# Kernel optimization log

Hardware: AMD Instinct MI355X
Metric: run time of the kernel (lower is better)

Reference implementation:

```python
import jax, jax.numpy as jnp
import numpy as np

B, D, C, NS = 4, 64, 16, 4          # batch (clusters), spatial size, nPlanes (constant mode), num_strides
LEAK, EPS = 0.0, 1e-4               # leakiness_enc, SCN BatchNorm eps
N = 200_000                          # total points across clusters
DN = ('NCDHW', 'DHWIO', 'NCDHW')


def _conv(x, w, stride=1, pad='SAME'):
    return jax.lax.conv_general_dilated(x, w, (stride,) * 3, pad, dimension_numbers=DN)


def _bn_lrelu(x, m, gamma, beta):
    # BatchNormLeakyReLU over ACTIVE sites only (mask m is {0,1} float [B,1,d,d,d])
    n = jnp.maximum(jnp.sum(m), 1.0)
    mean = jnp.sum(x * m, axis=(0, 2, 3, 4)) / n
    xc = x - mean[None, :, None, None, None]
    var = jnp.sum((xc * xc) * m, axis=(0, 2, 3, 4)) / n
    xh = xc * jax.lax.rsqrt(var + EPS)[None, :, None, None, None]
    xh = xh * gamma[None, :, None, None, None] + beta[None, :, None, None, None]
    return jnp.where(xh > 0, xh, LEAK * xh) * m


def _down_mask(m):
    # SCN strided Convolution: output site active if any input site in its 2x2x2 window is active
    d = m.shape[2]
    return m.reshape(B, 1, d // 2, 2, d // 2, 2, d // 2, 2).max(axis=(3, 5, 7))


def setup_inputs() -> dict:
    key = jax.random.key(0)
    ks = jax.random.split(key, 12)
    coords = jax.random.randint(ks[0], (N, 3), 0, D).astype(jnp.float32)
    data = jnp.concatenate([coords, jnp.zeros((N, 2), jnp.float32)], axis=1)  # cols 3,4 overwritten in fwd
    clust_ids = jax.random.randint(ks[1], (N,), 0, B)
    s = 0.1
    return {
        'data': data,
        'clust_ids': clust_ids,
        'w_prep': jax.random.normal(ks[2], (3, 3, 3, 1, C)) * s,
        'enc_gamma': jnp.ones((NS - 1, C)),
        'enc_beta': jnp.zeros((NS - 1, C)),
        'enc_wsub': jax.random.normal(ks[3], (NS - 1, 3, 3, 3, C, C)) * s,
        'enc_wdown': jax.random.normal(ks[4], (NS - 1, 2, 2, 2, C, C)) * s,
        'dec_gamma': jnp.ones((NS - 1, C)),
        'dec_beta': jnp.zeros((NS - 1, C)),
        'dec_wup': jax.random.normal(ks[5], (NS - 1, 2, 2, 2, C, C)) * s,
        'dec_wsub3': jax.random.normal(ks[6], (NS - 1, 3, 3, 3, C, C)) * s,
        'dec_wsub4': jax.random.normal(ks[7], (NS - 1, 4, 4, 4, C, C)) * s,
        'w_out': jax.random.normal(ks[8], (3, 3, 3, C, 1)) * s,
    }


def reference(data, clust_ids, w_prep, enc_gamma, enc_beta, enc_wsub, enc_wdown,
              dec_gamma, dec_beta, dec_wup, dec_wsub3, dec_wsub4, w_out):
    # --- InputLayer (mode=3: sum duplicate coords); features are all ones ---
    ijk = data[:, :3].astype(jnp.int32)
    b = clust_ids.astype(jnp.int32)
    lin = ((b * D + ijk[:, 0]) * D + ijk[:, 1]) * D + ijk[:, 2]
    x = jnp.zeros((B * D * D * D,), jnp.float32).at[lin].add(1.0).reshape(B, 1, D, D, D)
    mask = (x > 0).astype(jnp.float32)  # active-site mask (submanifold semantics)

    # prepare: SubmanifoldConvolution(1 -> C, k=3, no bias)
    x = _conv(x, w_prep) * mask

    # encoder
    masks = []
    for i in range(NS - 1):
        masks.append(mask)
        x = _bn_lrelu(x, mask, enc_gamma[i], enc_beta[i])
        x = _conv(x, enc_wsub[i]) * mask                      # submanifold k=3
        x = _conv(x, enc_wdown[i], stride=2, pad='VALID')      # strided Convolution k=2 s=2
        mask = _down_mask(mask)
        x = x * mask
    # last encoder stage is an empty Sequential (identity)

    hidden = x.reshape(B, -1)  # SparseToDense + view: [B, C*(D/2^(NS-1))^3]

    # decoder
    for j in range(NS - 1):
        lvl = NS - 2 - j
        x = _bn_lrelu(x, mask, dec_gamma[j], dec_beta[j])
        mask = masks[lvl]  # FullConvolution restores encoder-level active set
        x = jax.lax.conv_transpose(x, dec_wup[j], (2, 2, 2), 'VALID', dimension_numbers=DN) * mask
        x = _conv(x, dec_wsub3[j]) * mask                      # submanifold k=3
        # SparsifyFCS: keep sites where feature channel 0 > 0 (applied twice; idempotent)
        mask = mask * (x[:, :1] > 0).astype(jnp.float32)
        x = x * mask
        x = _conv(x, dec_wsub4[j], pad=[(1, 2)] * 3) * mask    # submanifold k=4

    out = _conv(x, w_out) * mask                               # output: SubmanifoldConvolution(C -> 1, k=3)
    return hidden, out
```

## Files before the change

### kernel.cpp

```cpp
#include <hip/hip_runtime.h>

#define TPB 256
#define CTPB 512

__device__ __forceinline__ void fma4(float4& a, float s, const float4 b){
  a.x = fmaf(s,b.x,a.x); a.y = fmaf(s,b.y,a.y);
  a.z = fmaf(s,b.z,a.z); a.w = fmaf(s,b.w,a.w);
}

__device__ __forceinline__ int vox(int b,int z,int y,int x,int ld){
  return ((((((b<<ld)|z)<<ld)|y)<<ld)|x);
}

__device__ __forceinline__ float chan(const float4&a0,const float4&a1,const float4&a2,const float4&a3,int c){
  const float4& f = (c<4)?a0:((c<8)?a1:((c<12)?a2:a3));
  int r=c&3;
  return r==0?f.x:(r==1?f.y:(r==2?f.z:f.w));
}

__device__ __forceinline__ void append_list(bool a, int v, int* __restrict__ list, int* __restrict__ cnt){
  __shared__ int lcnt, lbase;
  __shared__ int woff[TPB/64];
  if(threadIdx.x==0) lcnt=0;
  __syncthreads();
  unsigned long long bl = __ballot(a);
  int lane = threadIdx.x & 63;
  int wv = threadIdx.x >> 6;
  if(lane==0){ int pop=__popcll(bl); woff[wv] = pop ? atomicAdd(&lcnt,pop) : 0; }
  __syncthreads();
  if(threadIdx.x==0 && lcnt) lbase = atomicAdd(cnt, lcnt);
  __syncthreads();
  if(a) list[lbase + woff[wv] + __popcll(bl & ((1ull<<lane)-1ull))] = v;
}

__device__ __forceinline__ void stats_reduce(const float4&a0,const float4&a1,const float4&a2,const float4&a3,
                                             float* red, float* __restrict__ gsums){
  int lane=threadIdx.x&63, wv=threadIdx.x>>6, nw=blockDim.x>>6;
  #pragma unroll
  for(int c=0;c<16;c++){
    float x = chan(a0,a1,a2,a3,c);
    float q = x*x;
    for(int o=32;o>0;o>>=1){ x+=__shfl_down(x,o,64); q+=__shfl_down(q,o,64); }
    if(lane==0){ red[wv*32+c]=x; red[wv*32+16+c]=q; }
  }
  __syncthreads();
  if(threadIdx.x<32){
    float t=0.f;
    for(int w=0;w<nw;w++) t+=red[w*32+threadIdx.x];
    atomicAdd(&gsums[threadIdx.x], t);
  }
}

__device__ __forceinline__ void stats_reduce4(const float4&a, float* red, float* __restrict__ gsums){
  int lane=threadIdx.x&63, wv=threadIdx.x>>6, nw=blockDim.x>>6;
  float sx[4]={a.x,a.y,a.z,a.w};
  float sq[4]={a.x*a.x,a.y*a.y,a.z*a.z,a.w*a.w};
  for(int o=32;o>=4;o>>=1){
    #pragma unroll
    for(int k=0;k<4;k++){ sx[k]+=__shfl_down(sx[k],o,64); sq[k]+=__shfl_down(sq[k],o,64); }
  }
  if(lane<4){
    #pragma unroll
    for(int k=0;k<4;k++){ red[wv*32+lane*4+k]=sx[k]; red[wv*32+16+lane*4+k]=sq[k]; }
  }
  __syncthreads();
  if(threadIdx.x<32){
    float t=0.f;
    for(int w=0;w<nw;w++) t+=red[w*32+threadIdx.x];
    atomicAdd(&gsums[threadIdx.x], t);
  }
}

__global__ __launch_bounds__(TPB) void k_scatter(const float* __restrict__ data, const int* __restrict__ cl,
                                                 int n, float* __restrict__ c0){
  int i = blockIdx.x*blockDim.x + threadIdx.x;
  if(i>=n) return;
  int z=(int)data[i*5+0], y=(int)data[i*5+1], x=(int)data[i*5+2];
  atomicAdd(&c0[vox(cl[i],z,y,x,6)], 1.0f);
}

__global__ __launch_bounds__(TPB) void k_cnt0(const float* __restrict__ c0, int n, int* __restrict__ bc){
  int i = blockIdx.x*TPB + threadIdx.x;
  bool a = (i<n) && (c0[i]>0.f);
  unsigned long long bl = __ballot(a);
  __shared__ int wcnt[TPB/64];
  int lane=threadIdx.x&63, wv=threadIdx.x>>6;
  if(lane==0) wcnt[wv]=__popcll(bl);
  __syncthreads();
  if(threadIdx.x==0) bc[blockIdx.x]=wcnt[0]+wcnt[1]+wcnt[2]+wcnt[3];
}

__global__ __launch_bounds__(1024) void k_scan0(int* __restrict__ bc, int nb, int* __restrict__ total){
  __shared__ int s[1024];
  int t=threadIdx.x, b4=t*4;
  int v0 = (b4+0<nb)?bc[b4+0]:0;
  int v1 = (b4+1<nb)?bc[b4+1]:0;
  int v2 = (b4+2<nb)?bc[b4+2]:0;
  int v3 = (b4+3<nb)?bc[b4+3]:0;
  int sum=v0+v1+v2+v3;
  s[t]=sum; __syncthreads();
  for(int o=1;o<1024;o<<=1){
    int x = (t>=o)? s[t-o] : 0;
    __syncthreads();
    s[t]+=x;
    __syncthreads();
  }
  int excl=s[t]-sum;
  if(b4+0<nb) bc[b4+0]=excl;
  if(b4+1<nb) bc[b4+1]=excl+v0;
  if(b4+2<nb) bc[b4+2]=excl+v0+v1;
  if(b4+3<nb) bc[b4+3]=excl+v0+v1+v2;
  if(t==1023) *total = s[1023];
}

__global__ __launch_bounds__(TPB) void k_emit0(const float* __restrict__ c0, int n,
                                               const int* __restrict__ bc, int* __restrict__ list){
  int i = blockIdx.x*TPB + threadIdx.x;
  bool a = (i<n) && (c0[i]>0.f);
  unsigned long long bl = __ballot(a);
  __shared__ int woff[TPB/64];
  __shared__ int wpre[TPB/64];
  int lane=threadIdx.x&63, wv=threadIdx.x>>6;
  if(lane==0) woff[wv]=__popcll(bl);
  __syncthreads();
  if(threadIdx.x==0){ int acc=0; for(int w=0;w<TPB/64;w++){ wpre[w]=acc; acc+=woff[w]; } }
  __syncthreads();
  if(a) list[bc[blockIdx.x] + wpre[wv] + __popcll(bl&((1ull<<lane)-1ull))] = i;
}

__global__ __launch_bounds__(TPB) void k_markparent_compact(const int* __restrict__ listF, const int* __restrict__ cntF,
        int ldf, int* __restrict__ g, int* __restrict__ listC, int* __restrict__ cntC){
  int i = blockIdx.x*TPB + threadIdx.x;
  bool first=false; int p=0;
  if(i < *cntF){
    int v=listF[i];
    int dm=(1<<ldf)-1;
    int x=v&dm, y=(v>>ldf)&dm, z=(v>>(2*ldf))&dm, b=v>>(3*ldf);
    p=vox(b,z>>1,y>>1,x>>1,ldf-1);
    first = (atomicExch(&g[p],1)==0);
  }
  append_list(first,p,listC,cntC);
}

__global__ __launch_bounds__(TPB) void k_sparsify_compact(float* __restrict__ X, float* __restrict__ Y,
        const int* __restrict__ listA, const int* __restrict__ cntA,
        int* __restrict__ listB, int* __restrict__ cntB, int* __restrict__ gmask){
  int i = blockIdx.x*TPB + threadIdx.x;
  bool keep=false; int v=0;
  if(i < *cntA){
    v = listA[i];
    keep = X[(size_t)v<<4] > 0.f;
    if(!keep){
      float4 zz = make_float4(0,0,0,0);
      float4* px=(float4*)(X+((size_t)v<<4)); px[0]=zz;px[1]=zz;px[2]=zz;px[3]=zz;
      float4* py=(float4*)(Y+((size_t)v<<4)); py[0]=zz;py[1]=zz;py[2]=zz;py[3]=zz;
      if(gmask) gmask[v]=0;
    }
  }
  append_list(keep,v,listB,cntB);
}

__global__ __launch_bounds__(TPB) void k_prep_l(const float* __restrict__ c0, const int* __restrict__ list,
          const int* __restrict__ cnt, const float* __restrict__ w, float* __restrict__ X,
          float* __restrict__ gsums){
  __shared__ float wl[432];
  __shared__ float red[(TPB/64)*32];
  for(int i=threadIdx.x;i<432;i+=TPB) wl[i]=w[i];
  __syncthreads();
  int i = blockIdx.x*TPB + threadIdx.x;
  bool act = i < *cnt;
  float4 a0=make_float4(0,0,0,0), a1=a0, a2=a0, a3=a0;
  if(act){
    int v=list[i];
    int x=v&63, y=(v>>6)&63, z=(v>>12)&63, b=v>>18;
    for(int dz=0;dz<3;dz++){ int zz=z+dz-1; if((unsigned)zz>=64u) continue;
      for(int dy=0;dy<3;dy++){ int yy=y+dy-1; if((unsigned)yy>=64u) continue;
        for(int dx=0;dx<3;dx++){ int xx=x+dx-1; if((unsigned)xx>=64u) continue;
          float av = c0[vox(b,zz,yy,xx,6)];
          if(av==0.f) continue;
          const float4* wv=(const float4*)&wl[((dz*3+dy)*3+dx)<<4];
          fma4(a0,av,wv[0]); fma4(a1,av,wv[1]); fma4(a2,av,wv[2]); fma4(a3,av,wv[3]);
        }
      }
    }
    float4* o=(float4*)(X+((size_t)v<<4));
    o[0]=a0;o[1]=a1;o[2]=a2;o[3]=a3;
  }
  stats_reduce(a0,a1,a2,a3,red,gsums);
}

__global__ __launch_bounds__(CTPB) void k_conv3_l(const float* __restrict__ Xin, const int* __restrict__ list,
      const int* __restrict__ cnt, const float* __restrict__ w, const int* __restrict__ actg,
      float* __restrict__ Xout, int ld){
  __shared__ float wl[6912];
  int nwork = *cnt;
  if((int)((blockIdx.x*CTPB)>>2) >= nwork) return;
  for(int i=threadIdx.x;i<6912;i+=CTPB) wl[i]=w[i];
  __syncthreads();
  int t = blockIdx.x*CTPB + threadIdx.x;
  int i = t>>2, sub = t&3;
  if(i >= nwork) return;
  int v = list[i];
  int d=1<<ld, dm=d-1;
  int x=v&dm, y=(v>>ld)&dm, z=(v>>(2*ld))&dm, b=v>>(3*ld);
  float4 acc=make_float4(0,0,0,0);
  for(int dz=0;dz<3;dz++){ int zz=z+dz-1; if((unsigned)zz>=(unsigned)d) continue;
    for(int dy=0;dy<3;dy++){ int yy=y+dy-1; if((unsigned)yy>=(unsigned)d) continue;
      int rb = vox(b,zz,yy,0,ld);
      const float* srow = Xin + ((size_t)rb<<4);
      const int* arow = actg + rb;
      int m[3];
      #pragma unroll
      for(int dx=0;dx<3;dx++){ int xx=x+dx-1; m[dx] = ((unsigned)xx<(unsigned)d) ? arow[xx] : 0; }
      const float* wrow = &wl[(((dz*3+dy)*3)<<8) + (sub<<2)];
      #pragma unroll
      for(int dx=0;dx<3;dx++){
        if(!m[dx]) continue;
        int xx=x+dx-1;
        const float4* sp=(const float4*)(srow + ((size_t)xx<<4));
        float s[16];
        *(float4*)&s[0]=sp[0]; *(float4*)&s[4]=sp[1]; *(float4*)&s[8]=sp[2]; *(float4*)&s[12]=sp[3];
        const float* wt = wrow + (dx<<8);
        #pragma unroll
        for(int ci=0;ci<16;ci++)
          fma4(acc, s[ci], *(const float4*)(wt + (ci<<4)));
      }
    }
  }
  ((float4*)(Xout + ((size_t)v<<4)))[sub] = acc;
}

__global__ __launch_bounds__(CTPB) void k_conv4_l(const float* __restrict__ Xin, const int* __restrict__ list,
      const int* __restrict__ cnt, const float* __restrict__ w, const int* __restrict__ actg,
      float* __restrict__ Xout, int ld, float* __restrict__ gsums){
  __shared__ float wl[8192];
  __shared__ float red[(CTPB/64)*32];
  int nwork = *cnt;
  if((int)((blockIdx.x*CTPB)>>2) >= nwork) return;
  int t = blockIdx.x*CTPB + threadIdx.x;
  int i = t>>2, sub = t&3;
  bool act = i < nwork;
  int v=0,x=0,y=0,z=0,b=0,d=1<<ld,dm=d-1;
  if(act){
    v = list[i];
    x=v&dm; y=(v>>ld)&dm; z=(v>>(2*ld))&dm; b=v>>(3*ld);
  }
  float4 acc=make_float4(0,0,0,0);
  for(int half=0;half<2;half++){
    __syncthreads();
    for(int k=threadIdx.x;k<8192;k+=CTPB) wl[k]=w[half*8192+k];
    __syncthreads();
    if(act){
      for(int dzl=0;dzl<2;dzl++){ int dz=half*2+dzl;
        int zz=z+dz-1; if((unsigned)zz>=(unsigned)d) continue;
        for(int dy=0;dy<4;dy++){ int yy=y+dy-1; if((unsigned)yy>=(unsigned)d) continue;
          int rb = vox(b,zz,yy,0,ld);
          const float* srow = Xin + ((size_t)rb<<4);
          const int* arow = actg + rb;
          int m[4];
          #pragma unroll
          for(int dx=0;dx<4;dx++){ int xx=x+dx-1; m[dx] = ((unsigned)xx<(unsigned)d) ? arow[xx] : 0; }
          const float* wrow = &wl[((dzl*4+dy)<<10) + (sub<<2)];
          #pragma unroll
          for(int dx=0;dx<4;dx++){
            if(!m[dx]) continue;
            int xx=x+dx-1;
            const float4* sp=(const float4*)(srow + ((size_t)xx<<4));
            float s[16];
            *(float4*)&s[0]=sp[0]; *(float4*)&s[4]=sp[1]; *(float4*)&s[8]=sp[2]; *(float4*)&s[12]=sp[3];
            const float* wt = wrow + (dx<<8);
            #pragma unroll
            for(int ci=0;ci<16;ci++)
              fma4(acc, s[ci], *(const float4*)(wt + (ci<<4)));
          }
        }
      }
    }
  }
  if(act) ((float4*)(Xout + ((size_t)v<<4)))[sub] = acc;
  __syncthreads();
  stats_reduce4(acc, red, gsums);
}

__global__ __launch_bounds__(TPB) void k_down_l(const float* __restrict__ Xin, const int* __restrict__ list,
      const int* __restrict__ cnt, const float* __restrict__ w, const int* __restrict__ actf,
      float* __restrict__ Xout, int ldc, float* __restrict__ gsums){
  __shared__ float wl[2048];
  __shared__ float red[(TPB/64)*32];
  int nwork = *cnt;
  for(int k=threadIdx.x;k<2048;k+=TPB) wl[k]=w[k];
  __syncthreads();
  int t = blockIdx.x*TPB + threadIdx.x;
  int i = t>>2, sub = t&3;
  bool act = i < nwork;
  float4 acc=make_float4(0,0,0,0);
  if(act){
    int v = list[i];
    int dm=(1<<ldc)-1, ldf=ldc+1;
    int x=v&dm, y=(v>>ldc)&dm, z=(v>>(2*ldc))&dm, b=v>>(3*ldc);
    for(int dz=0;dz<2;dz++) for(int dy=0;dy<2;dy++) for(int dx=0;dx<2;dx++){
      int fi = vox(b,2*z+dz,2*y+dy,2*x+dx,ldf);
      if(!actf[fi]) continue;
      const float4* sp=(const float4*)(Xin + ((size_t)fi<<4));
      float s[16];
      *(float4*)&s[0]=sp[0]; *(float4*)&s[4]=sp[1]; *(float4*)&s[8]=sp[2]; *(float4*)&s[12]=sp[3];
      const float* wt=&wl[((((dz<<1)|dy)<<1 | dx)<<8) + (sub<<2)];
      #pragma unroll
      for(int ci=0;ci<16;ci++)
        fma4(acc, s[ci], *(const float4*)(wt+(ci<<4)));
    }
    ((float4*)(Xout+((size_t)v<<4)))[sub] = acc;
  }
  stats_reduce4(acc, red, gsums);
}

__global__ __launch_bounds__(TPB) void k_upbn_l(const float* __restrict__ Xc, const int* __restrict__ list,
      const int* __restrict__ cnt, const float* __restrict__ w,
      const float* __restrict__ sums, const int* __restrict__ bncnt,
      const float* __restrict__ g, const float* __restrict__ bta,
      const int* __restrict__ gmask, float* __restrict__ Xf, int ldf){
  __shared__ float wl[2048];
  __shared__ float sc[16], sh[16];
  for(int k=threadIdx.x;k<2048;k+=TPB) wl[k]=w[k];
  if(threadIdx.x<16){
    int c=threadIdx.x;
    float n=(float)(*bncnt); if(n<1.f) n=1.f;
    float mean=sums[c]/n;
    float var=sums[16+c]/n - mean*mean;
    float s=g[c]/sqrtf(var+1e-4f);
    sc[c]=s; sh[c]=fmaf(-mean,s,bta[c]);
  }
  __syncthreads();
  int i = blockIdx.x*TPB + threadIdx.x;
  if(i >= *cnt) return;
  int v = list[i];
  int dm=(1<<ldf)-1, ldc=ldf-1;
  int x=v&dm, y=(v>>ldf)&dm, z=(v>>(2*ldf))&dm, b=v>>(3*ldf);
  int p = vox(b,z>>1,y>>1,x>>1,ldc);
  float4 a0=make_float4(0,0,0,0), a1=a0, a2=a0, a3=a0;
  if(gmask[p]!=0){
    const float4* sp=(const float4*)(Xc + ((size_t)p<<4));
    float s[16];
    *(float4*)&s[0]=sp[0]; *(float4*)&s[4]=sp[1]; *(float4*)&s[8]=sp[2]; *(float4*)&s[12]=sp[3];
    #pragma unroll
    for(int ci=0;ci<16;ci++){ float xh=fmaf(s[ci],sc[ci],sh[ci]); s[ci]=xh>0.f?xh:0.f; }
    int tpar = ((((z&1)^1)<<1 | ((y&1)^1))<<1) | ((x&1)^1);
    const float* wt=&wl[tpar<<8];
    #pragma unroll
    for(int ci=0;ci<16;ci++){
      float av=s[ci];
      const float4* wv=(const float4*)(wt+(ci<<4));
      fma4(a0,av,wv[0]); fma4(a1,av,wv[1]); fma4(a2,av,wv[2]); fma4(a3,av,wv[3]);
    }
  }
  float4* o=(float4*)(Xf+((size_t)v<<4));
  o[0]=a0;o[1]=a1;o[2]=a2;o[3]=a3;
}

__global__ __launch_bounds__(TPB) void k_bnapply(float* __restrict__ X, const int* __restrict__ list,
        const int* __restrict__ cnt, const float* __restrict__ sums,
        const float* __restrict__ g, const float* __restrict__ bta){
  __shared__ float sc[16], sh[16];
  if(threadIdx.x<16){
    int c=threadIdx.x;
    float n=(float)(*cnt); if(n<1.f) n=1.f;
    float mean=sums[c]/n;
    float var=sums[16+c]/n - mean*mean;
    float s=g[c]/sqrtf(var+1e-4f);
    sc[c]=s; sh[c]=fmaf(-mean,s,bta[c]);
  }
  __syncthreads();
  int i = blockIdx.x*TPB + threadIdx.x;
  if(i>=*cnt) return;
  float* p = X + ((size_t)list[i]<<4);
  #pragma unroll
  for(int c=0;c<16;c++){
    float xh = fmaf(p[c], sc[c], sh[c]);
    p[c] = xh>0.f ? xh : 0.f;
  }
}

__global__ __launch_bounds__(TPB) void k_hidden(const float* __restrict__ X3, float* __restrict__ out){
  int i = blockIdx.x*TPB + threadIdx.x;
  if(i>=4*8192) return;
  int b=i>>13, r=i&8191, c=r>>9, s=r&511;
  out[i] = X3[(((size_t)((b<<9)|s))<<4)|c];
}

__global__ __launch_bounds__(TPB) void k_final_l(const float* __restrict__ Xin, const int* __restrict__ list,
      const int* __restrict__ cnt, const float* __restrict__ w, const int* __restrict__ actg,
      float* __restrict__ out){
  __shared__ float wl[432];
  for(int k=threadIdx.x;k<432;k+=TPB) wl[k]=w[k];
  __syncthreads();
  int i = blockIdx.x*TPB + threadIdx.x;
  if(i >= *cnt) return;
  int v = list[i];
  float acc=0.f;
  int x=v&63, y=(v>>6)&63, z=(v>>12)&63, b=v>>18;
  for(int dz=0;dz<3;dz++){ int zz=z+dz-1; if((unsigned)zz>=64u) continue;
    for(int dy=0;dy<3;dy++){ int yy=y+dy-1; if((unsigned)yy>=64u) continue;
      int rb = vox(b,zz,yy,0,6);
      const int* arow = actg + rb;
      int m[3];
      #pragma unroll
      for(int dx=0;dx<3;dx++){ int xx=x+dx-1; m[dx] = ((unsigned)xx<64u) ? arow[xx] : 0; }
      #pragma unroll
      for(int dx=0;dx<3;dx++){
        if(!m[dx]) continue;
        int xx=x+dx-1;
        const float* sp = Xin + ((size_t)(rb+xx)<<4);
        const float* wt = &wl[((dz*3+dy)*3+dx)<<4];
        #pragma unroll
        for(int ci=0;ci<16;ci++) acc = fmaf(sp[ci], wt[ci], acc);
      }
    }
  }
  out[v]=acc;
}

static inline int nb(int n){ return (n+TPB-1)/TPB; }
static inline int nbC(int n){ return (n+CTPB-1)/CTPB; }
static inline size_t rbytes(int ld){ return ((size_t)4<<(3*ld))*64; }

extern "C" void kernel_launch(void* const* d_in, const int* in_sizes, int n_in,
                              void* d_out, int out_size, void* d_ws, size_t ws_size,
                              hipStream_t stream){
  const float* data   = (const float*)d_in[0];
  const int*   cl     = (const int*)d_in[1];
  const float* w_prep = (const float*)d_in[2];
  const float* enc_g  = (const float*)d_in[3];
  const float* enc_b  = (const float*)d_in[4];
  const float* enc_ws = (const float*)d_in[5];
  const float* enc_wd = (const float*)d_in[6];
  const float* dec_g  = (const float*)d_in[7];
  const float* dec_b  = (const float*)d_in[8];
  const float* dec_wu = (const float*)d_in[9];
  const float* dec_w3 = (const float*)d_in[10];
  const float* dec_w4 = (const float*)d_in[11];
  const float* w_out  = (const float*)d_in[12];
  int N = in_sizes[0]/5;
  float* outp = (float*)d_out;

  const size_t FEAT_ROOMY = 38305792;
  const size_t FEAT_TIGHT = 33554432;
  const size_t TAILN      = 1048576 + 149504 + 224 + 16 + 4096 + 821248;
  bool roomy = ws_size >= (FEAT_ROOMY + TAILN)*sizeof(float);

  float* ws = (float*)d_ws;
  float *A[4]={0,0,0,0}, *B[4]={0,0,0,0}, *X=0, *Y=0;
  size_t featsz;
  if(roomy){
    A[0]=ws;            B[0]=A[0]+16777216;
    A[1]=B[0]+16777216; B[1]=A[1]+2097152;
    A[2]=B[1]+2097152;  B[2]=A[2]+262144;
    A[3]=B[2]+262144;
    featsz=FEAT_ROOMY;
  } else { X=ws; Y=X+16777216; featsz=FEAT_TIGHT; }
  float* c0 = ws + featsz;
  int* g1=(int*)(c0+1048576); int* g2=g1+131072; int* g3=g2+16384;
  float* sums=(float*)(g3+2048);
  int* counts=(int*)(sums+224);
  int* bc=counts+16;
  int* l0a=bc+4096; int* l0b=l0a+262144; int* l1a=l0b+262144; int* l1b=l1a+131072;
  int* l2a=l1b+131072; int* l2b=l2a+16384; int* l3=l2b+16384;
  int* la[4]={l0a,l1a,l2a,l3};
  int* lb[3]={l0b,l1b,l2b};
  int* g[4]={nullptr,g1,g2,g3};
  int* actF[4]={(int*)c0, g1, g2, g3};
  int b0 = N<262144?N:262144;
  int bounds[4]={b0,131072,16384,2048};

  if(roomy){
    hipMemsetAsync(A[3], 0, 32768*sizeof(float), stream);
  } else {
    hipMemsetAsync(ws, 0, featsz*sizeof(float), stream);
  }
  hipMemsetAsync(c0, 0, (1048576+149504+224+16+4096)*sizeof(float), stream);

  k_scatter<<<nb(N),TPB,0,stream>>>(data, cl, N, c0);
  k_cnt0 <<<4096,TPB,0,stream>>>(c0, 1048576, bc);
  k_scan0<<<1,1024,0,stream>>>(bc, 4096, counts+0);
  k_emit0<<<4096,TPB,0,stream>>>(c0, 1048576, bc, l0a);

  if(roomy){
    k_prep_l<<<nb(b0),TPB,0,stream>>>(c0, l0a, counts+0, w_prep, A[0], sums);
    for(int i=0;i<3;i++){
      int ld=6-i;
      k_bnapply<<<nb(bounds[i]),TPB,0,stream>>>(A[i], la[i], counts+i, sums+32*i, enc_g+16*i, enc_b+16*i);
      k_conv3_l<<<nbC(4*bounds[i]),CTPB,0,stream>>>(A[i], la[i], counts+i, enc_ws+6912*i, actF[i], B[i], ld);
      k_markparent_compact<<<nb(bounds[i]),TPB,0,stream>>>(la[i], counts+i, ld, g[i+1], la[i+1], counts+(i+1));
      k_down_l<<<nb(4*bounds[i+1]),TPB,0,stream>>>(B[i], la[i+1], counts+(i+1), enc_wd+2048*i, actF[i], A[i+1], ld-1, sums+32*(i+1));
    }
    k_hidden<<<nb(32768),TPB,0,stream>>>(A[3], outp);
    for(int j=0;j<3;j++){
      int lvl=2-j, ldf=6-lvl;
      const int* bncnt = (j==0)? counts+3 : counts+4+(lvl+1);
      k_upbn_l<<<nb(bounds[lvl]),TPB,0,stream>>>(A[lvl+1], la[lvl], counts+lvl, dec_wu+2048*j,
            sums+32*(3+j), bncnt, dec_g+16*j, dec_b+16*j, g[lvl+1], A[lvl], ldf);
      k_conv3_l<<<nbC(4*bounds[lvl]),CTPB,0,stream>>>(A[lvl], la[lvl], counts+lvl, dec_w3+6912*j, actF[lvl], B[lvl], ldf);
      k_sparsify_compact<<<nb(bounds[lvl]),TPB,0,stream>>>(B[lvl], A[lvl], la[lvl], counts+lvl, lb[lvl], counts+4+lvl, g[lvl]);
      float* ss = (j<2)? sums+32*(4+j) : sums+32*6;
      k_conv4_l<<<nbC(4*bounds[lvl]),CTPB,0,stream>>>(B[lvl], lb[lvl], counts+4+lvl, dec_w4+16384*j, actF[lvl], A[lvl], ldf, ss);
    }
    hipMemsetAsync(outp+32768, 0, (size_t)1048576*sizeof(float), stream);
    k_final_l<<<nb(b0),TPB,0,stream>>>(A[0], lb[0], counts+4, w_out, actF[0], outp+32768);
  } else {
    k_prep_l<<<nb(b0),TPB,0,stream>>>(c0, l0a, counts+0, w_prep, X, sums);
    float* cur=X; float* oth=Y; int ld=6;
    for(int i=0;i<3;i++){
      k_bnapply<<<nb(bounds[i]),TPB,0,stream>>>(cur, la[i], counts+i, sums+32*i, enc_g+16*i, enc_b+16*i);
      hipMemsetAsync(oth, 0, rbytes(ld), stream);
      k_conv3_l<<<nbC(4*bounds[i]),CTPB,0,stream>>>(cur, la[i], counts+i, enc_ws+6912*i, actF[i], oth, ld);
      { float* t=cur; cur=oth; oth=t; }
      k_markparent_compact<<<nb(bounds[i]),TPB,0,stream>>>(la[i], counts+i, ld, g[i+1], la[i+1], counts+(i+1));
      hipMemsetAsync(oth, 0, rbytes(ld-1), stream);
      k_down_l<<<nb(4*bounds[i+1]),TPB,0,stream>>>(cur, la[i+1], counts+(i+1), enc_wd+2048*i, actF[i], oth, ld-1, sums+32*(i+1));
      { float* t=cur; cur=oth; oth=t; }
      ld--;
    }
    k_hidden<<<nb(32768),TPB,0,stream>>>(cur, outp);
    for(int j=0;j<3;j++){
      int lvl=2-j, ldf=ld+1;
      const int* bncnt = (j==0)? counts+3 : counts+4+(lvl+1);
      hipMemsetAsync(oth, 0, rbytes(ldf), stream);
      k_upbn_l<<<nb(bounds[lvl]),TPB,0,stream>>>(cur, la[lvl], counts+lvl, dec_wu+2048*j,
            sums+32*(3+j), bncnt, dec_g+16*j, dec_b+16*j, g[lvl+1], oth, ldf);
      { float* t=cur; cur=oth; oth=t; }
      hipMemsetAsync(oth, 0, rbytes(ldf), stream);
      k_conv3_l<<<nbC(4*bounds[lvl]),CTPB,0,stream>>>(cur, la[lvl], counts+lvl, dec_w3+6912*j, actF[lvl], oth, ldf);
      { float* t=cur; cur=oth; oth=t; }
      k_sparsify_compact<<<nb(bounds[lvl]),TPB,0,stream>>>(cur, oth, la[lvl], counts+lvl, lb[lvl], counts+4+lvl, g[lvl]);
      float* ss = (j<2)? sums+32*(4+j) : sums+32*6;
      k_conv4_l<<<nbC(4*bounds[lvl]),CTPB,0,stream>>>(cur, lb[lvl], counts+4+lvl, dec_w4+16384*j, actF[lvl], oth, ldf, ss);
      { float* t=cur; cur=oth; oth=t; }
      ld=ldf;
    }
    hipMemsetAsync(outp+32768, 0, (size_t)1048576*sizeof(float), stream);
    k_final_l<<<nb(b0),TPB,0,stream>>>(cur, lb[0], counts+4, w_out, actF[0], outp+32768);
  }
}
```

Measured before the change: 726.5 us.

## Precompute per-site neighbor tap bitmasks to replace dense active-grid lookups in convs

Builds 64-bit row occupancy bitmaps for each level, from the emit ballot at level 0 and a new row-bits kernel for the coarser levels. A new kernel uses them to compute per-site 3x3x3 and 4x4x4 neighbor tap masks. The conv3, conv4 and final kernels then skip empty taps and rows using these masks, instead of loading the dense int active grid for every neighbor. Sparsify carries the masks into the compacted list. The masks can be stale after sparsification, but removed sites were already zeroed, so results stay correct. The cost is extra kernel launches and extra workspace memory.

```diff
diff --git a/kernel.cpp b/kernel.cpp
--- a/kernel.cpp
+++ b/kernel.cpp
@@ -2,6 +2,8 @@
 
 #define TPB 256
 #define CTPB 512
+
+typedef unsigned long long ull;
 
 __device__ __forceinline__ void fma4(float4& a, float s, const float4 b){
   a.x = fmaf(s,b.x,a.x); a.y = fmaf(s,b.y,a.y);
@@ -18,7 +20,7 @@
   return r==0?f.x:(r==1?f.y:(r==2?f.z:f.w));
 }
 
-__device__ __forceinline__ void append_list(bool a, int v, int* __restrict__ list, int* __restrict__ cnt){
+__device__ __forceinline__ int append_list(bool a, int v, int* __restrict__ list, int* __restrict__ cnt){
   __shared__ int lcnt, lbase;
   __shared__ int woff[TPB/64];
   if(threadIdx.x==0) lcnt=0;
@@ -30,7 +32,12 @@
   __syncthreads();
   if(threadIdx.x==0 && lcnt) lbase = atomicAdd(cnt, lcnt);
   __syncthreads();
-  if(a) list[lbase + woff[wv] + __popcll(bl & ((1ull<<lane)-1ull))] = v;
+  int pos = -1;
+  if(a){
+    pos = lbase + woff[wv] + __popcll(bl & ((1ull<<lane)-1ull));
+    list[pos] = v;
+  }
+  return pos;
 }
 
 __device__ __forceinline__ void stats_reduce(const float4&a0,const float4&a1,const float4&a2,const float4&a3,
@@ -114,18 +121,51 @@
 }
 
 __global__ __launch_bounds__(TPB) void k_emit0(const float* __restrict__ c0, int n,
-                                               const int* __restrict__ bc, int* __restrict__ list){
+                                               const int* __restrict__ bc, int* __restrict__ list,
+                                               ull* __restrict__ rowb){
   int i = blockIdx.x*TPB + threadIdx.x;
   bool a = (i<n) && (c0[i]>0.f);
   unsigned long long bl = __ballot(a);
   __shared__ int woff[TPB/64];
   __shared__ int wpre[TPB/64];
   int lane=threadIdx.x&63, wv=threadIdx.x>>6;
-  if(lane==0) woff[wv]=__popcll(bl);
+  if(lane==0){ woff[wv]=__popcll(bl); rowb[i>>6]=bl; }
   __syncthreads();
   if(threadIdx.x==0){ int acc=0; for(int w=0;w<TPB/64;w++){ wpre[w]=acc; acc+=woff[w]; } }
   __syncthreads();
   if(a) list[bc[blockIdx.x] + wpre[wv] + __popcll(bl&((1ull<<lane)-1ull))] = i;
+}
+
+__global__ __launch_bounds__(TPB) void k_rowbits(const int* __restrict__ g, int d, int nrows,
+                                                 ull* __restrict__ out){
+  int r = blockIdx.x*TPB + threadIdx.x;
+  if(r>=nrows) return;
+  const int* base = g + r*d;
+  ull w=0;
+  for(int x=0;x<d;x++) if(base[x]) w |= (1ull<<x);
+  out[r]=w;
+}
+
+__global__ __launch_bounds__(TPB) void k_tapmask(const int* __restrict__ list, const int* __restrict__ cnt,
+        const ull* __restrict__ rowb, int ld, int* __restrict__ tm3, ull* __restrict__ tm4){
+  int i = blockIdx.x*TPB + threadIdx.x;
+  if(i>=*cnt) return;
+  int v = list[i];
+  int d=1<<ld, dm=d-1;
+  int x=v&dm, y=(v>>ld)&dm, z=(v>>(2*ld))&dm, b=v>>(3*ld);
+  ull t4=0; int t3=0;
+  for(int oz=-1;oz<=2;oz++){
+    int zz=z+oz; if((unsigned)zz>=(unsigned)d) continue;
+    for(int oy=-1;oy<=2;oy++){
+      int yy=y+oy; if((unsigned)yy>=(unsigned)d) continue;
+      ull row = rowb[vox(b,zz,yy,0,ld)>>ld];
+      ull w = (x>=1) ? (row>>(x-1)) : (row<<1);
+      int dz=oz+1, dy=oy+1;
+      t4 |= (w & 0xFull) << (((dz<<2)|dy)<<2);
+      if(oz<=1 && oy<=1) t3 |= ((int)(w & 7ull)) << ((dz*3+dy)*3);
+    }
+  }
+  tm3[i]=t3; tm4[i]=t4;
 }
 
 __global__ __launch_bounds__(TPB) void k_markparent_compact(const int* __restrict__ listF, const int* __restrict__ cntF,
@@ -144,7 +184,9 @@
 
 __global__ __launch_bounds__(TPB) void k_sparsify_compact(float* __restrict__ X, float* __restrict__ Y,
         const int* __restrict__ listA, const int* __restrict__ cntA,
-        int* __restrict__ listB, int* __restrict__ cntB, int* __restrict__ gmask){
+        int* __restrict__ listB, int* __restrict__ cntB, int* __restrict__ gmask,
+        const int* __restrict__ tm3a, const ull* __restrict__ tm4a,
+        int* __restrict__ tm3b, ull* __restrict__ tm4b){
   int i = blockIdx.x*TPB + threadIdx.x;
   bool keep=false; int v=0;
   if(i < *cntA){
@@ -157,7 +199,8 @@
       if(gmask) gmask[v]=0;
     }
   }
-  append_list(keep,v,listB,cntB);
+  int pos = append_list(keep,v,listB,cntB);
+  if(keep){ tm3b[pos]=tm3a[i]; tm4b[pos]=tm4a[i]; }
 }
 
 __global__ __launch_bounds__(TPB) void k_prep_l(const float* __restrict__ c0, const int* __restrict__ list,
@@ -190,7 +233,7 @@
 }
 
 __global__ __launch_bounds__(CTPB) void k_conv3_l(const float* __restrict__ Xin, const int* __restrict__ list,
-      const int* __restrict__ cnt, const float* __restrict__ w, const int* __restrict__ actg,
+      const int* __restrict__ cnt, const float* __restrict__ w, const int* __restrict__ tm3,
       float* __restrict__ Xout, int ld){
   __shared__ float wl[6912];
   int nwork = *cnt;
@@ -201,23 +244,22 @@
   int i = t>>2, sub = t&3;
   if(i >= nwork) return;
   int v = list[i];
-  int d=1<<ld, dm=d-1;
+  int tmv = tm3[i];
+  int dm=(1<<ld)-1;
   int x=v&dm, y=(v>>ld)&dm, z=(v>>(2*ld))&dm, b=v>>(3*ld);
   float4 acc=make_float4(0,0,0,0);
-  for(int dz=0;dz<3;dz++){ int zz=z+dz-1; if((unsigned)zz>=(unsigned)d) continue;
-    for(int dy=0;dy<3;dy++){ int yy=y+dy-1; if((unsigned)yy>=(unsigned)d) continue;
-      int rb = vox(b,zz,yy,0,ld);
-      const float* srow = Xin + ((size_t)rb<<4);
-      const int* arow = actg + rb;
-      int m[3];
-      #pragma unroll
-      for(int dx=0;dx<3;dx++){ int xx=x+dx-1; m[dx] = ((unsigned)xx<(unsigned)d) ? arow[xx] : 0; }
+  for(int dz=0;dz<3;dz++){
+    int rz=(tmv>>(9*dz))&511; if(!rz) continue;
+    int zz=z+dz-1;
+    for(int dy=0;dy<3;dy++){
+      int rm=(rz>>(3*dy))&7; if(!rm) continue;
+      int yy=y+dy-1;
+      const float* srow = Xin + ((size_t)vox(b,zz,yy,0,ld)<<4);
       const float* wrow = &wl[(((dz*3+dy)*3)<<8) + (sub<<2)];
       #pragma unroll
       for(int dx=0;dx<3;dx++){
-        if(!m[dx]) continue;
-        int xx=x+dx-1;
-        const float4* sp=(const float4*)(srow + ((size_t)xx<<4));
+        if(!(rm&(1<<dx))) continue;
+        const float4* sp=(const float4*)(srow + ((size_t)(x+dx-1)<<4));
         float s[16];
         *(float4*)&s[0]=sp[0]; *(float4*)&s[4]=sp[1]; *(float4*)&s[8]=sp[2]; *(float4*)&s[12]=sp[3];
         const float* wt = wrow + (dx<<8);
@@ -231,7 +273,7 @@
 }
 
 __global__ __launch_bounds__(CTPB) void k_conv4_l(const float* __restrict__ Xin, const int* __restrict__ list,
-      const int* __restrict__ cnt, const float* __restrict__ w, const int* __restrict__ actg,
+      const int* __restrict__ cnt, const float* __restrict__ w, const ull* __restrict__ tm4,
       float* __restrict__ Xout, int ld, float* __restrict__ gsums){
   __shared__ float wl[8192];
   __shared__ float red[(CTPB/64)*32];
@@ -240,9 +282,11 @@
   int t = blockIdx.x*CTPB + threadIdx.x;
   int i = t>>2, sub = t&3;
   bool act = i < nwork;
-  int v=0,x=0,y=0,z=0,b=0,d=1<<ld,dm=d-1;
+  int v=0,x=0,y=0,z=0,b=0,dm=(1<<ld)-1;
+  ull tmv=0;
   if(act){
     v = list[i];
+    tmv = tm4[i];
     x=v&dm; y=(v>>ld)&dm; z=(v>>(2*ld))&dm; b=v>>(3*ld);
   }
   float4 acc=make_float4(0,0,0,0);
@@ -251,21 +295,21 @@
     for(int k=threadIdx.x;k<8192;k+=CTPB) wl[k]=w[half*8192+k];
     __syncthreads();
     if(act){
-      for(int dzl=0;dzl<2;dzl++){ int dz=half*2+dzl;
-        int zz=z+dz-1; if((unsigned)zz>=(unsigned)d) continue;
-        for(int dy=0;dy<4;dy++){ int yy=y+dy-1; if((unsigned)yy>=(unsigned)d) continue;
-          int rb = vox(b,zz,yy,0,ld);
-          const float* srow = Xin + ((size_t)rb<<4);
-          const int* arow = actg + rb;
-          int m[4];
-          #pragma unroll
-          for(int dx=0;dx<4;dx++){ int xx=x+dx-1; m[dx] = ((unsigned)xx<(unsigned)d) ? arow[xx] : 0; }
+      unsigned hw = (unsigned)(tmv >> (half*32));
+      for(int dzl=0;dzl<2;dzl++){
+        unsigned r16 = (hw>>(dzl*16)) & 0xFFFFu;
+        if(!r16) continue;
+        int zz = z + half*2 + dzl - 1;
+        for(int dy=0;dy<4;dy++){
+          unsigned m4 = (r16>>(dy*4)) & 0xFu;
+          if(!m4) continue;
+          int yy=y+dy-1;
+          const float* srow = Xin + ((size_t)vox(b,zz,yy,0,ld)<<4);
           const float* wrow = &wl[((dzl*4+dy)<<10) + (sub<<2)];
           #pragma unroll
           for(int dx=0;dx<4;dx++){
-            if(!m[dx]) continue;
-            int xx=x+dx-1;
-            const float4* sp=(const float4*)(srow + ((size_t)xx<<4));
+            if(!(m4&(1u<<dx))) continue;
+            const float4* sp=(const float4*)(srow + ((size_t)(x+dx-1)<<4));
             float s[16];
             *(float4*)&s[0]=sp[0]; *(float4*)&s[4]=sp[1]; *(float4*)&s[8]=sp[2]; *(float4*)&s[12]=sp[3];
             const float* wt = wrow + (dx<<8);
@@ -388,7 +432,7 @@
 }
 
 __global__ __launch_bounds__(TPB) void k_final_l(const float* __restrict__ Xin, const int* __restrict__ list,
-      const int* __restrict__ cnt, const float* __restrict__ w, const int* __restrict__ actg,
+      const int* __restrict__ cnt, const float* __restrict__ w, const int* __restrict__ tm3,
       float* __restrict__ out){
   __shared__ float wl[432];
   for(int k=threadIdx.x;k<432;k+=TPB) wl[k]=w[k];
@@ -396,20 +440,20 @@
   int i = blockIdx.x*TPB + threadIdx.x;
   if(i >= *cnt) return;
   int v = list[i];
+  int tmv = tm3[i];
   float acc=0.f;
   int x=v&63, y=(v>>6)&63, z=(v>>12)&63, b=v>>18;
-  for(int dz=0;dz<3;dz++){ int zz=z+dz-1; if((unsigned)zz>=64u) continue;
-    for(int dy=0;dy<3;dy++){ int yy=y+dy-1; if((unsigned)yy>=64u) continue;
+  for(int dz=0;dz<3;dz++){
+    int rz=(tmv>>(9*dz))&511; if(!rz) continue;
+    int zz=z+dz-1;
+    for(int dy=0;dy<3;dy++){
+      int rm=(rz>>(3*dy))&7; if(!rm) continue;
+      int yy=y+dy-1;
       int rb = vox(b,zz,yy,0,6);
-      const int* arow = actg + rb;
-      int m[3];
-      #pragma unroll
-      for(int dx=0;dx<3;dx++){ int xx=x+dx-1; m[dx] = ((unsigned)xx<64u) ? arow[xx] : 0; }
       #pragma unroll
       for(int dx=0;dx<3;dx++){
-        if(!m[dx]) continue;
-        int xx=x+dx-1;
-        const float* sp = Xin + ((size_t)(rb+xx)<<4);
+        if(!(rm&(1<<dx))) continue;
+        const float* sp = Xin + ((size_t)(rb+x+dx-1)<<4);
         const float* wt = &wl[((dz*3+dy)*3+dx)<<4];
         #pragma unroll
         for(int ci=0;ci<16;ci++) acc = fmaf(sp[ci], wt[ci], acc);
@@ -444,7 +488,7 @@
 
   const size_t FEAT_ROOMY = 38305792;
   const size_t FEAT_TIGHT = 33554432;
-  const size_t TAILN      = 1048576 + 149504 + 224 + 16 + 4096 + 821248;
+  const size_t TAILN      = 1048576 + 149504 + 224 + 16 + 4096 + 821248 + 2500608;
   bool roomy = ws_size >= (FEAT_ROOMY + TAILN)*sizeof(float);
 
   float* ws = (float*)d_ws;
@@ -464,10 +508,32 @@
   int* bc=counts+16;
   int* l0a=bc+4096; int* l0b=l0a+262144; int* l1a=l0b+262144; int* l1b=l1a+131072;
   int* l2a=l1b+131072; int* l2b=l2a+16384; int* l3=l2b+16384;
+  int* tail = l3+2048;
+  ull* rb0=(ull*)tail;
+  ull* rb1=rb0+16384;
+  ull* rb2=rb1+4096;
+  ull* tm4_0=rb2+1024;
+  ull* tm4_1=tm4_0+262144;
+  ull* tm4_2=tm4_1+131072;
+  ull* tm4b_0=tm4_2+16384;
+  ull* tm4b_1=tm4b_0+262144;
+  ull* tm4b_2=tm4b_1+131072;
+  int* tm3_0=(int*)(tm4b_2+16384);
+  int* tm3_1=tm3_0+262144;
+  int* tm3_2=tm3_1+131072;
+  int* tm3b_0=tm3_2+16384;
+  int* tm3b_1=tm3b_0+262144;
+  int* tm3b_2=tm3b_1+131072;
+
   int* la[4]={l0a,l1a,l2a,l3};
   int* lb[3]={l0b,l1b,l2b};
   int* g[4]={nullptr,g1,g2,g3};
   int* actF[4]={(int*)c0, g1, g2, g3};
+  ull* rbL[3]={rb0,rb1,rb2};
+  ull* tm4L[3]={tm4_0,tm4_1,tm4_2};
+  ull* tm4bL[3]={tm4b_0,tm4b_1,tm4b_2};
+  int* tm3L[3]={tm3_0,tm3_1,tm3_2};
+  int* tm3bL[3]={tm3b_0,tm3b_1,tm3b_2};
   int b0 = N<262144?N:262144;
   int bounds[4]={b0,131072,16384,2048};
 
@@ -481,15 +547,21 @@
   k_scatter<<<nb(N),TPB,0,stream>>>(data, cl, N, c0);
   k_cnt0 <<<4096,TPB,0,stream>>>(c0, 1048576, bc);
   k_scan0<<<1,1024,0,stream>>>(bc, 4096, counts+0);
-  k_emit0<<<4096,TPB,0,stream>>>(c0, 1048576, bc, l0a);
+  k_emit0<<<4096,TPB,0,stream>>>(c0, 1048576, bc, l0a, rb0);
+  k_tapmask<<<nb(b0),TPB,0,stream>>>(l0a, counts+0, rb0, 6, tm3L[0], tm4L[0]);
 
   if(roomy){
     k_prep_l<<<nb(b0),TPB,0,stream>>>(c0, l0a, counts+0, w_prep, A[0], sums);
     for(int i=0;i<3;i++){
       int ld=6-i;
       k_bnapply<<<nb(bounds[i]),TPB,0,stream>>>(A[i], la[i], counts+i, sums+32*i, enc_g+16*i, enc_b+16*i);
-      k_conv3_l<<<nbC(4*bounds[i]),CTPB,0,stream>>>(A[i], la[i], counts+i, enc_ws+6912*i, actF[i], B[i], ld);
+      k_conv3_l<<<nbC(4*bounds[i]),CTPB,0,stream>>>(A[i], la[i], counts+i, enc_ws+6912*i, tm3L[i], B[i], ld);
       k_markparent_compact<<<nb(bounds[i]),TPB,0,stream>>>(la[i], counts+i, ld, g[i+1], la[i+1], counts+(i+1));
+      if(i<2){
+        int dc=1<<(5-i), nrows=4*dc*dc;
+        k_rowbits<<<nb(nrows),TPB,0,stream>>>(g[i+1], dc, nrows, rbL[i+1]);
+        k_tapmask<<<nb(bounds[i+1]),TPB,0,stream>>>(la[i+1], counts+(i+1), rbL[i+1], 5-i, tm3L[i+1], tm4L[i+1]);
+      }
       k_down_l<<<nb(4*bounds[i+1]),TPB,0,stream>>>(B[i], la[i+1], counts+(i+1), enc_wd+2048*i, actF[i], A[i+1], ld-1, sums+32*(i+1));
     }
     k_hidden<<<nb(32768),TPB,0,stream>>>(A[3], outp);
@@ -498,22 +570,28 @@
       const int* bncnt = (j==0)? counts+3 : counts+4+(lvl+1);
       k_upbn_l<<<nb(bounds[lvl]),TPB,0,stream>>>(A[lvl+1], la[lvl], counts+lvl, dec_wu+2048*j,
             sums+32*(3+j), bncnt, dec_g+16*j, dec_b+16*j, g[lvl+1], A[lvl], ldf);
-      k_conv3_l<<<nbC(4*bounds[lvl]),CTPB,0,stream>>>(A[lvl], la[lvl], counts+lvl, dec_w3+6912*j, actF[lvl], B[lvl], ldf);
-      k_sparsify_compact<<<nb(bounds[lvl]),TPB,0,stream>>>(B[lvl], A[lvl], la[lvl], counts+lvl, lb[lvl], counts+4+lvl, g[lvl]);
+      k_conv3_l<<<nbC(4*bounds[lvl]),CTPB,0,stream>>>(A[lvl], la[lvl], counts+lvl, dec_w3+6912*j, tm3L[lvl], B[lvl], ldf);
+      k_sparsify_compact<<<nb(bounds[lvl]),TPB,0,stream>>>(B[lvl], A[lvl], la[lvl], counts+lvl, lb[lvl], counts+4+lvl, g[lvl],
+            tm3L[lvl], tm4L[lvl], tm3bL[lvl], tm4bL[lvl]);
       float* ss = (j<2)? sums+32*(4+j) : sums+32*6;
-      k_conv4_l<<<nbC(4*bounds[lvl]),CTPB,0,stream>>>(B[lvl], lb[lvl], counts+4+lvl, dec_w4+16384*j, actF[lvl], A[lvl], ldf, ss);
+      k_conv4_l<<<nbC(4*bounds[lvl]),CTPB,0,stream>>>(B[lvl], lb[lvl], counts+4+lvl, dec_w4+16384*j, tm4bL[lvl], A[lvl], ldf, ss);
     }
     hipMemsetAsync(outp+32768, 0, (size_t)1048576*sizeof(float), stream);
-    k_final_l<<<nb(b0),TPB,0,stream>>>(A[0], lb[0], counts+4, w_out, actF[0], outp+32768);
+    k_final_l<<<nb(b0),TPB,0,stream>>>(A[0], lb[0], counts+4, w_out, tm3bL[0], outp+32768);
   } else {
     k_prep_l<<<nb(b0),TPB,0,stream>>>(c0, l0a, counts+0, w_prep, X, sums);
     float* cur=X; float* oth=Y; int ld=6;
     for(int i=0;i<3;i++){
       k_bnapply<<<nb(bounds[i]),TPB,0,stream>>>(cur, la[i], counts+i, sums+32*i, enc_g+16*i, enc_b+16*i);
       hipMemsetAsync(oth, 0, rbytes(ld), stream);
-      k_conv3_l<<<nbC(4*bounds[i]),CTPB,0,stream>>>(cur, la[i], counts+i, enc_ws+6912*i, actF[i], oth, ld);
+      k_conv3_l<<<nbC(4*bounds[i]),CTPB,0,stream>>>(cur, la[i], counts+i, enc_ws+6912*i, tm3L[i], oth, ld);
       { float* t=cur; cur=oth; oth=t; }
       k_markparent_compact<<<nb(bounds[i]),TPB,0,stream>>>(la[i], counts+i, ld, g[i+1], la[i+1], counts+(i+1));
+      if(i<2){
+        int dc=1<<(5-i), nrows=4*dc*dc;
+        k_rowbits<<<nb(nrows),TPB,0,stream>>>(g[i+1], dc, nrows, rbL[i+1]);
+        k_tapmask<<<nb(bounds[i+1]),TPB,0,stream>>>(la[i+1], counts+(i+1), rbL[i+1], 5-i, tm3L[i+1], tm4L[i+1]);
+      }
       hipMemsetAsync(oth, 0, rbytes(ld-1), stream);
       k_down_l<<<nb(4*bounds[i+1]),TPB,0,stream>>>(cur, la[i+1], counts+(i+1), enc_wd+2048*i, actF[i], oth, ld-1, sums+32*(i+1));
       { float* t=cur; cur=oth; oth=t; }
@@ -528,15 +606,16 @@
             sums+32*(3+j), bncnt, dec_g+16*j, dec_b+16*j, g[lvl+1], oth, ldf);
       { float* t=cur; cur=oth; oth=t; }
       hipMemsetAsync(oth, 0, rbytes(ldf), stream);
-      k_conv3_l<<<nbC(4*bounds[lvl]),CTPB,0,stream>>>(cur, la[lvl], counts+lvl, dec_w3+6912*j, actF[lvl], oth, ldf);
+      k_conv3_l<<<nbC(4*bounds[lvl]),CTPB,0,stream>>>(cur, la[lvl], counts+lvl, dec_w3+6912*j, tm3L[lvl], oth, ldf);
       { float* t=cur; cur=oth; oth=t; }
-      k_sparsify_compact<<<nb(bounds[lvl]),TPB,0,stream>>>(cur, oth, la[lvl], counts+lvl, lb[lvl], counts+4+lvl, g[lvl]);
+      k_sparsify_compact<<<nb(bounds[lvl]),TPB,0,stream>>>(cur, oth, la[lvl], counts+lvl, lb[lvl], counts+4+lvl, g[lvl],
+            tm3L[lvl], tm4L[lvl], tm3bL[lvl], tm4bL[lvl]);
       float* ss = (j<2)? sums+32*(4+j) : sums+32*6;
-      k_conv4_l<<<nbC(4*bounds[lvl]),CTPB,0,stream>>>(cur, lb[lvl], counts+4+lvl, dec_w4+16384*j, actF[lvl], oth, ldf, ss);
+      k_conv4_l<<<nbC(4*bounds[lvl]),CTPB,0,stream>>>(cur, lb[lvl], counts+4+lvl, dec_w4+16384*j, tm4bL[lvl], oth, ldf, ss);
       { float* t=cur; cur=oth; oth=t; }
       ld=ldf;
     }
     hipMemsetAsync(outp+32768, 0, (size_t)1048576*sizeof(float), stream);
-    k_final_l<<<nb(b0),TPB,0,stream>>>(cur, lb[0], counts+4, w_out, actF[0], outp+32768);
-  }
-}
+    k_final_l<<<nb(b0),TPB,0,stream>>>(cur, lb[0], counts+4, w_out, tm3bL[0], outp+32768);
+  }
+}
```

After: 638.5 us, median of 2. -12.1%, faster.
